# Kernel optimization log

Measured on AMD Instinct MI355X. Metric: run time of the kernel, lower is better.

Reference implementation:

```python
import jax, jax.numpy as jnp
import numpy as np

B, S, D, H = 2, 2048, 1024, 16  # batch, seq, embed_dim, num_heads
DH = D // H                      # head dim = 64


def setup_inputs() -> dict:
    key = jax.random.key(0)
    kx, kq, kbq, kk, kbk, kv, kbv = jax.random.split(key, 7)
    scale = 1.0 / np.sqrt(D)
    return {
        "x": jax.random.normal(kx, (B, S, D), dtype=jnp.float32),
        "Wq": jax.random.normal(kq, (D, D), dtype=jnp.float32) * scale,
        "bq": jax.random.normal(kbq, (D,), dtype=jnp.float32) * 0.01,
        "Wk": jax.random.normal(kk, (D, D), dtype=jnp.float32) * scale,
        "bk": jax.random.normal(kbk, (D,), dtype=jnp.float32) * 0.01,
        "Wv": jax.random.normal(kv, (D, D), dtype=jnp.float32) * scale,
        "bv": jax.random.normal(kbv, (D,), dtype=jnp.float32) * 0.01,
    }


def reference(x, Wq, bq, Wk, bk, Wv, bv):
    # ooqkv_type == 'q', odeint_method == 'id': q branch = act(Linear(x)), exact GELU (torch nn.GELU default)
    q = jax.nn.gelu(x @ Wq + bq, approximate=False)
    k = x @ Wk + bk
    v = x @ Wv + bv
    # [B, S, D] -> [B, S, H, DH]
    q = q.reshape(B, S, H, DH)
    k = k.reshape(B, S, H, DH)
    v = v.reshape(B, S, H, DH)
    # NOTE: original module has NO 1/sqrt(d) scale — faithful reproduction
    att = jnp.einsum("bqhd,bkhd->bhqk", q, k)
    att = jax.nn.softmax(att, axis=-1)
    out = jnp.einsum("bhqk,bkhd->bqhd", att, v)
    return out.reshape(B, S, D)
```

## Files before the change

kernel.cpp:

```cpp
#include <hip/hip_runtime.h>
#include <math.h>

#define B_  2
#define S_  2048
#define D_  1024
#define H_  16
#define DH_ 64
#define M_  (B_ * S_)

typedef _Float16 half_t;
typedef __attribute__((ext_vector_type(8))) _Float16 h8;
typedef __attribute__((ext_vector_type(4))) _Float16 h4;
typedef __attribute__((ext_vector_type(4))) float   f32x4;

#define LOG2E 1.44269504088896f

__device__ __forceinline__ void gll16(const half_t* g, half_t* l) {
    __builtin_amdgcn_global_load_lds(
        (__attribute__((address_space(1))) const void*)g,
        (__attribute__((address_space(3))) void*)l, 16, 0, 0);
}

__global__ __launch_bounds__(256) void prep_k(
    const float* __restrict__ x, half_t* __restrict__ xh,
    const float* __restrict__ Wq, const float* __restrict__ Wk,
    const float* __restrict__ Wv, half_t* __restrict__ Wt)
{
    const int bx = blockIdx.x;
    if (bx < 2048) {
        const size_t i = ((size_t)bx * 256 + threadIdx.x) * 8;
        const float4 a = *(const float4*)(x + i);
        const float4 b = *(const float4*)(x + i + 4);
        h8 o;
        o[0] = (half_t)a.x; o[1] = (half_t)a.y; o[2] = (half_t)a.z; o[3] = (half_t)a.w;
        o[4] = (half_t)b.x; o[5] = (half_t)b.y; o[6] = (half_t)b.z; o[7] = (half_t)b.w;
        *(h8*)(xh + i) = o;
    } else {
        const int gb    = bx - 2048;
        const int which = gb >> 9;
        const float* __restrict__ W = (which == 0) ? Wq : (which == 1) ? Wk : Wv;
        half_t* __restrict__ T = Wt + (size_t)which * D_ * D_;
        const int gw   = (gb & 511) * 4 + (threadIdx.x >> 6);
        const int lane = threadIdx.x & 63;
        const int n    = (gw & 15) * 64 + lane;
        const int k0   = (gw >> 4) * 8;
        h8 o;
        #pragma unroll
        for (int t = 0; t < 8; ++t) o[t] = (half_t)W[(size_t)(k0 + t) * D_ + n];
        *(h8*)(T + (size_t)n * D_ + k0) = o;
    }
}

__global__ __launch_bounds__(256) void qkv_gemm_f16(
    const half_t* __restrict__ xh, const half_t* __restrict__ Wt,
    const float* __restrict__ bq, const float* __restrict__ bk,
    const float* __restrict__ bv,
    half_t* __restrict__ Qo, half_t* __restrict__ Ko, half_t* __restrict__ Vt)
{
    const int n0g   = blockIdx.x * 128;
    const int which = n0g >> 10;
    const int n0    = n0g & 1023;
    const int m0    = blockIdx.y * 128;
    const half_t* __restrict__ Wp  = Wt + (size_t)which * D_ * D_;
    const float* __restrict__ bias = (which == 0) ? bq : (which == 1) ? bk : bv;

    const int tid = threadIdx.x, lane = tid & 63, wave = tid >> 6;
    const int wm = (wave >> 1) * 64, wn = (wave & 1) * 64;
    const int ln = lane & 15, quad = lane >> 4;

    __shared__ __align__(16) half_t As[128 * 64];
    __shared__ __align__(16) half_t Bs[128 * 64];

    f32x4 acc[4][4];
    #pragma unroll
    for (int i = 0; i < 4; ++i)
        #pragma unroll
        for (int j = 0; j < 4; ++j) acc[i][j] = (f32x4){0.f, 0.f, 0.f, 0.f};

    for (int k0 = 0; k0 < D_; k0 += 64) {
        __syncthreads();
        #pragma unroll
        for (int l = 0; l < 4; ++l) {
            const int c  = tid + l * 256;
            const int r  = c >> 3, c0 = c & 7;
            const int cs = c0 ^ (r & 7);
            gll16(xh + (size_t)(m0 + r) * D_ + k0 + cs * 8, &As[c * 8]);
            gll16(Wp + (size_t)(n0 + r) * D_ + k0 + cs * 8, &Bs[c * 8]);
        }
        __syncthreads();

        #pragma unroll
        for (int kc = 0; kc < 2; ++kc) {
            h8 af[4], bf[4];
            #pragma unroll
            for (int i = 0; i < 4; ++i) {
                const int r = wm + i * 16 + ln;
                af[i] = *(const h8*)&As[r * 64 + (((kc << 2) + quad) ^ (r & 7)) * 8];
            }
            #pragma unroll
            for (int j = 0; j < 4; ++j) {
                const int r = wn + j * 16 + ln;
                bf[j] = *(const h8*)&Bs[r * 64 + (((kc << 2) + quad) ^ (r & 7)) * 8];
            }
            #pragma unroll
            for (int i = 0; i < 4; ++i)
                #pragma unroll
                for (int j = 0; j < 4; ++j)
                    acc[i][j] = __builtin_amdgcn_mfma_f32_16x16x32_f16(
                        af[i], bf[j], acc[i][j], 0, 0, 0);
        }
    }

    if (which == 2) {
        #pragma unroll
        for (int j = 0; j < 4; ++j) {
            const int col = n0 + wn + j * 16 + ln;
            const int h = col >> 6, d = col & 63;
            const float bb = bias[col];
            #pragma unroll
            for (int i = 0; i < 4; ++i) {
                const int sg = m0 + wm + i * 16 + quad * 4;
                const int b  = sg >> 11, srow = sg & 2047;
                h4 pv;
                #pragma unroll
                for (int r = 0; r < 4; ++r) pv[r] = (half_t)(acc[i][j][r] + bb);
                *(h4*)(Vt + (((size_t)(b * H_ + h) * DH_ + d) * S_ + srow)) = pv;
            }
        }
    } else {
        half_t* __restrict__ out = (which == 0) ? Qo : Ko;
        #pragma unroll
        for (int j = 0; j < 4; ++j) {
            const int col = n0 + wn + j * 16 + ln;
            const float bb = bias[col];
            #pragma unroll
            for (int i = 0; i < 4; ++i) {
                #pragma unroll
                for (int r = 0; r < 4; ++r) {
                    const int row = m0 + wm + i * 16 + quad * 4 + r;
                    float t = acc[i][j][r] + bb;
                    if (which == 0) {
                        const float u = t * fmaf(t * t, 0.0356774081f, 0.7978845608f);
                        const float e = __builtin_amdgcn_exp2f(u * -2.88539008178f);
                        t = t * __builtin_amdgcn_rcpf(1.0f + e) * LOG2E;
                    }
                    out[(size_t)row * D_ + col] = (half_t)t;
                }
            }
        }
    }
}

__global__ __launch_bounds__(512) void attn_f16(
    const half_t* __restrict__ Q, const half_t* __restrict__ K,
    const half_t* __restrict__ Vt, float* __restrict__ out)
{
    const int tid  = threadIdx.x;
    const int lane = tid & 63;
    const int wave = tid >> 6;
    const int ln   = lane & 15;
    const int quad = lane >> 4;
    const int bh   = blockIdx.y;
    const int b    = bh >> 4;
    const int h    = bh & 15;
    const int q0   = blockIdx.x * 128;

    const half_t* __restrict__ Qb  = Q  + (size_t)b * S_ * D_ + h * DH_;
    const half_t* __restrict__ Kb  = K  + (size_t)b * S_ * D_ + h * DH_;
    const half_t* __restrict__ Vtb = Vt + (size_t)bh * DH_ * S_;

    __shared__ __align__(16) half_t Ks[64 * 64];
    __shared__ __align__(16) half_t Vs[64 * 64];
    __shared__ __align__(16) half_t QPs[128][72];

    {
    }
    const int sr  = tid >> 3, sc0 = tid & 7;
    const int scs = sc0 ^ (sr & 7);
    const half_t* kSrc = Kb  + (size_t)sr * D_ + scs * 8;
    const half_t* vSrc = Vtb + (size_t)sr * S_ + scs * 8;
    half_t* const kDst = &Ks[tid * 8];
    half_t* const vDst = &Vs[tid * 8];

    #pragma unroll
    for (int l = 0; l < 2; ++l) {
        const int c = tid + l * 512;
        const int r = c >> 3, k8 = c & 7;
        *(h8*)&QPs[r][k8 * 8] = *(const h8*)(Qb + (size_t)(q0 + r) * D_ + k8 * 8);
    }
    __syncthreads();
    const h8 qa0 = *(const h8*)&QPs[wave * 16 + ln][quad * 8];
    const h8 qa1 = *(const h8*)&QPs[wave * 16 + ln][32 + quad * 8];

    h8 ones8;
    #pragma unroll
    for (int t = 0; t < 8; ++t) ones8[t] = (half_t)1.0f;

    f32x4 Oa[4];
    #pragma unroll
    for (int j = 0; j < 4; ++j) Oa[j] = (f32x4){0.f, 0.f, 0.f, 0.f};
    f32x4 la = (f32x4){0.f, 0.f, 0.f, 0.f};
    float m_a = -INFINITY;

    for (int k0 = 0; k0 < S_; k0 += 64) {
        __syncthreads();
        gll16(kSrc, kDst);
        gll16(vSrc, vDst);
        kSrc += 64 * D_;
        vSrc += 64;
        __syncthreads();

        f32x4 sa[4];
        __builtin_amdgcn_s_setprio(1);
        #pragma unroll
        for (int j = 0; j < 4; ++j) {
            const int rK = j * 16 + ln;
            const h8 ka0 = *(const h8*)&Ks[rK * 64 + ((quad)     ^ (rK & 7)) * 8];
            const h8 ka1 = *(const h8*)&Ks[rK * 64 + ((quad + 4) ^ (rK & 7)) * 8];
            f32x4 t = (f32x4){0.f, 0.f, 0.f, 0.f};
            t = __builtin_amdgcn_mfma_f32_16x16x32_f16(ka0, qa0, t, 0, 0, 0);
            t = __builtin_amdgcn_mfma_f32_16x16x32_f16(ka1, qa1, t, 0, 0, 0);
            sa[j] = t;
        }
        __builtin_amdgcn_s_setprio(0);

        float mxa = sa[0][0];
        #pragma unroll
        for (int j = 0; j < 4; ++j)
            #pragma unroll
            for (int r = 0; r < 4; ++r) mxa = fmaxf(mxa, sa[j][r]);
        mxa = fmaxf(mxa, __shfl_xor(mxa, 16, 64));
        mxa = fmaxf(mxa, __shfl_xor(mxa, 32, 64));

        if (__ballot(mxa > m_a)) {
            const float mna = fmaxf(m_a, mxa);
            const float ala = __builtin_amdgcn_exp2f(m_a - mna);
            m_a = mna;
            float ra[4];
            #pragma unroll
            for (int r = 0; r < 4; ++r) ra[r] = __shfl(ala, quad * 4 + r, 64);
            #pragma unroll
            for (int r = 0; r < 4; ++r) {
                la[r] *= ra[r];
                #pragma unroll
                for (int j = 0; j < 4; ++j) Oa[j][r] *= ra[r];
            }
        }

        #pragma unroll
        for (int j = 0; j < 4; ++j) {
            h4 pva;
            #pragma unroll
            for (int r = 0; r < 4; ++r)
                pva[r] = (half_t)__builtin_amdgcn_exp2f(sa[j][r] - m_a);
            *(h4*)&QPs[wave * 16 + ln][j * 16 + quad * 4] = pva;
        }

        const h8 pa0 = *(const h8*)&QPs[wave * 16 + ln][quad * 8];
        const h8 pa1 = *(const h8*)&QPs[wave * 16 + ln][32 + quad * 8];
        __builtin_amdgcn_s_setprio(1);
        #pragma unroll
        for (int j = 0; j < 4; ++j) {
            const int rV = j * 16 + ln;
            const h8 vb0 = *(const h8*)&Vs[rV * 64 + ((quad)     ^ (rV & 7)) * 8];
            const h8 vb1 = *(const h8*)&Vs[rV * 64 + ((quad + 4) ^ (rV & 7)) * 8];
            Oa[j] = __builtin_amdgcn_mfma_f32_16x16x32_f16(pa0, vb0, Oa[j], 0, 0, 0);
            Oa[j] = __builtin_amdgcn_mfma_f32_16x16x32_f16(pa1, vb1, Oa[j], 0, 0, 0);
        }
        la = __builtin_amdgcn_mfma_f32_16x16x32_f16(pa0, ones8, la, 0, 0, 0);
        la = __builtin_amdgcn_mfma_f32_16x16x32_f16(pa1, ones8, la, 0, 0, 0);
        __builtin_amdgcn_s_setprio(0);
    }

    #pragma unroll
    for (int r = 0; r < 4; ++r) {
        const float iva = 1.0f / la[r];
        const int rowa = q0 + wave * 16 + quad * 4 + r;
        #pragma unroll
        for (int j = 0; j < 4; ++j)
            out[((size_t)b * S_ + rowa) * D_ + h * DH_ + j * 16 + ln] = Oa[j][r] * iva;
    }
}

extern "C" void kernel_launch(void* const* d_in, const int* in_sizes, int n_in,
                              void* d_out, int out_size, void* d_ws, size_t ws_size,
                              hipStream_t stream) {
    const float* x  = (const float*)d_in[0];
    const float* Wq = (const float*)d_in[1];
    const float* bq = (const float*)d_in[2];
    const float* Wk = (const float*)d_in[3];
    const float* bk = (const float*)d_in[4];
    const float* Wv = (const float*)d_in[5];
    const float* bv = (const float*)d_in[6];
    float* out = (float*)d_out;

    const size_t nmd = (size_t)M_ * D_;
    const size_t ndd = (size_t)D_ * D_;
    half_t* xh  = (half_t*)d_ws;
    half_t* Wt  = xh + nmd;
    half_t* Qh  = Wt + 3 * ndd;
    half_t* Kh  = Qh + nmd;
    half_t* Vtw = Kh + nmd;

    prep_k<<<2048 + 1536, 256, 0, stream>>>(x, xh, Wq, Wk, Wv, Wt);
    qkv_gemm_f16<<<dim3(3 * D_ / 128, M_ / 128), 256, 0, stream>>>(
        xh, Wt, bq, bk, bv, Qh, Kh, Vtw);
    attn_f16<<<dim3(S_ / 128, B_ * H_), 512, 0, stream>>>(Qh, Kh, Vtw, out);
}
```

Measured before the change: 186.5 us.

## Double-buffer K/V tiles in attention kernel to overlap loads with compute

Splits the K/V shared-memory tiles into two ping-pong buffers and issues the async global-to-LDS load for the next tile before computing on the current one. This removes the serial load-then-wait step at the start of each key block, so memory latency can hide behind the MFMA and softmax work. The tile body moves into a macro that is invoked twice per unrolled iteration. In exchange it uses an extra 16 KB of LDS per block, which could lower occupancy, and the loop is hardcoded to 16 double-iterations.

```diff
diff --git a/kernel.cpp b/kernel.cpp
--- a/kernel.cpp
+++ b/kernel.cpp
@@ -151,6 +151,66 @@
     }
 }
 
+#define ATTN_TILE(KS, VS)                                                     \
+    do {                                                                      \
+        f32x4 sa[4];                                                          \
+        __builtin_amdgcn_s_setprio(1);                                        \
+        _Pragma("unroll")                                                     \
+        for (int j = 0; j < 4; ++j) {                                         \
+            const int rK = j * 16 + ln;                                       \
+            const h8 ka0 = *(const h8*)&KS[rK * 64 + ((quad)     ^ (rK & 7)) * 8]; \
+            const h8 ka1 = *(const h8*)&KS[rK * 64 + ((quad + 4) ^ (rK & 7)) * 8]; \
+            f32x4 t = (f32x4){0.f, 0.f, 0.f, 0.f};                            \
+            t = __builtin_amdgcn_mfma_f32_16x16x32_f16(ka0, qa0, t, 0, 0, 0); \
+            t = __builtin_amdgcn_mfma_f32_16x16x32_f16(ka1, qa1, t, 0, 0, 0); \
+            sa[j] = t;                                                        \
+        }                                                                     \
+        __builtin_amdgcn_s_setprio(0);                                        \
+        float mxa = sa[0][0];                                                 \
+        _Pragma("unroll")                                                     \
+        for (int j = 0; j < 4; ++j)                                           \
+            _Pragma("unroll")                                                 \
+            for (int r = 0; r < 4; ++r) mxa = fmaxf(mxa, sa[j][r]);           \
+        mxa = fmaxf(mxa, __shfl_xor(mxa, 16, 64));                            \
+        mxa = fmaxf(mxa, __shfl_xor(mxa, 32, 64));                            \
+        if (__ballot(mxa > m_a)) {                                            \
+            const float mna = fmaxf(m_a, mxa);                                \
+            const float ala = __builtin_amdgcn_exp2f(m_a - mna);              \
+            m_a = mna;                                                        \
+            float ra[4];                                                      \
+            _Pragma("unroll")                                                 \
+            for (int r = 0; r < 4; ++r) ra[r] = __shfl(ala, quad * 4 + r, 64);\
+            _Pragma("unroll")                                                 \
+            for (int r = 0; r < 4; ++r) {                                     \
+                la[r] *= ra[r];                                               \
+                _Pragma("unroll")                                             \
+                for (int j = 0; j < 4; ++j) Oa[j][r] *= ra[r];                \
+            }                                                                 \
+        }                                                                     \
+        _Pragma("unroll")                                                     \
+        for (int j = 0; j < 4; ++j) {                                         \
+            h4 pva;                                                           \
+            _Pragma("unroll")                                                 \
+            for (int r = 0; r < 4; ++r)                                       \
+                pva[r] = (half_t)__builtin_amdgcn_exp2f(sa[j][r] - m_a);      \
+            *(h4*)&QPs[wave * 16 + ln][j * 16 + quad * 4] = pva;              \
+        }                                                                     \
+        const h8 pa0 = *(const h8*)&QPs[wave * 16 + ln][quad * 8];            \
+        const h8 pa1 = *(const h8*)&QPs[wave * 16 + ln][32 + quad * 8];       \
+        __builtin_amdgcn_s_setprio(1);                                        \
+        _Pragma("unroll")                                                     \
+        for (int j = 0; j < 4; ++j) {                                         \
+            const int rV = j * 16 + ln;                                       \
+            const h8 vb0 = *(const h8*)&VS[rV * 64 + ((quad)     ^ (rV & 7)) * 8]; \
+            const h8 vb1 = *(const h8*)&VS[rV * 64 + ((quad + 4) ^ (rV & 7)) * 8]; \
+            Oa[j] = __builtin_amdgcn_mfma_f32_16x16x32_f16(pa0, vb0, Oa[j], 0, 0, 0); \
+            Oa[j] = __builtin_amdgcn_mfma_f32_16x16x32_f16(pa1, vb1, Oa[j], 0, 0, 0); \
+        }                                                                     \
+        la = __builtin_amdgcn_mfma_f32_16x16x32_f16(pa0, ones8, la, 0, 0, 0); \
+        la = __builtin_amdgcn_mfma_f32_16x16x32_f16(pa1, ones8, la, 0, 0, 0); \
+        __builtin_amdgcn_s_setprio(0);                                        \
+    } while (0)
+
 __global__ __launch_bounds__(512) void attn_f16(
     const half_t* __restrict__ Q, const half_t* __restrict__ K,
     const half_t* __restrict__ Vt, float* __restrict__ out)
@@ -169,18 +229,23 @@
     const half_t* __restrict__ Kb  = K  + (size_t)b * S_ * D_ + h * DH_;
     const half_t* __restrict__ Vtb = Vt + (size_t)bh * DH_ * S_;
 
-    __shared__ __align__(16) half_t Ks[64 * 64];
-    __shared__ __align__(16) half_t Vs[64 * 64];
+    __shared__ __align__(16) half_t Ks0[64 * 64];
+    __shared__ __align__(16) half_t Vs0[64 * 64];
+    __shared__ __align__(16) half_t Ks1[64 * 64];
+    __shared__ __align__(16) half_t Vs1[64 * 64];
     __shared__ __align__(16) half_t QPs[128][72];
 
-    {
-    }
     const int sr  = tid >> 3, sc0 = tid & 7;
     const int scs = sc0 ^ (sr & 7);
-    const half_t* kSrc = Kb  + (size_t)sr * D_ + scs * 8;
-    const half_t* vSrc = Vtb + (size_t)sr * S_ + scs * 8;
-    half_t* const kDst = &Ks[tid * 8];
-    half_t* const vDst = &Vs[tid * 8];
+    const half_t* kS = Kb  + (size_t)sr * D_ + scs * 8;
+    const half_t* vS = Vtb + (size_t)sr * S_ + scs * 8;
+    half_t* const kD0 = &Ks0[tid * 8];
+    half_t* const vD0 = &Vs0[tid * 8];
+    half_t* const kD1 = &Ks1[tid * 8];
+    half_t* const vD1 = &Vs1[tid * 8];
+
+    gll16(kS, kD0); gll16(vS, vD0);
+    kS += 64 * D_; vS += 64;
 
     #pragma unroll
     for (int l = 0; l < 2; ++l) {
@@ -202,74 +267,18 @@
     f32x4 la = (f32x4){0.f, 0.f, 0.f, 0.f};
     float m_a = -INFINITY;
 
-    for (int k0 = 0; k0 < S_; k0 += 64) {
+    for (int it = 0; it < 16; ++it) {
+        gll16(kS, kD1); gll16(vS, vD1);
+        kS += 64 * D_; vS += 64;
+        ATTN_TILE(Ks0, Vs0);
         __syncthreads();
-        gll16(kSrc, kDst);
-        gll16(vSrc, vDst);
-        kSrc += 64 * D_;
-        vSrc += 64;
+
+        if (it < 15) {
+            gll16(kS, kD0); gll16(vS, vD0);
+            kS += 64 * D_; vS += 64;
+        }
+        ATTN_TILE(Ks1, Vs1);
         __syncthreads();
-
-        f32x4 sa[4];
-        __builtin_amdgcn_s_setprio(1);
-        #pragma unroll
-        for (int j = 0; j < 4; ++j) {
-            const int rK = j * 16 + ln;
-            const h8 ka0 = *(const h8*)&Ks[rK * 64 + ((quad)     ^ (rK & 7)) * 8];
-            const h8 ka1 = *(const h8*)&Ks[rK * 64 + ((quad + 4) ^ (rK & 7)) * 8];
-            f32x4 t = (f32x4){0.f, 0.f, 0.f, 0.f};
-            t = __builtin_amdgcn_mfma_f32_16x16x32_f16(ka0, qa0, t, 0, 0, 0);
-            t = __builtin_amdgcn_mfma_f32_16x16x32_f16(ka1, qa1, t, 0, 0, 0);
-            sa[j] = t;
-        }
-        __builtin_amdgcn_s_setprio(0);
-
-        float mxa = sa[0][0];
-        #pragma unroll
-        for (int j = 0; j < 4; ++j)
-            #pragma unroll
-            for (int r = 0; r < 4; ++r) mxa = fmaxf(mxa, sa[j][r]);
-        mxa = fmaxf(mxa, __shfl_xor(mxa, 16, 64));
-        mxa = fmaxf(mxa, __shfl_xor(mxa, 32, 64));
-
-        if (__ballot(mxa > m_a)) {
-            const float mna = fmaxf(m_a, mxa);
-            const float ala = __builtin_amdgcn_exp2f(m_a - mna);
-            m_a = mna;
-            float ra[4];
-            #pragma unroll
-            for (int r = 0; r < 4; ++r) ra[r] = __shfl(ala, quad * 4 + r, 64);
-            #pragma unroll
-            for (int r = 0; r < 4; ++r) {
-                la[r] *= ra[r];
-                #pragma unroll
-                for (int j = 0; j < 4; ++j) Oa[j][r] *= ra[r];
-            }
-        }
-
-        #pragma unroll
-        for (int j = 0; j < 4; ++j) {
-            h4 pva;
-            #pragma unroll
-            for (int r = 0; r < 4; ++r)
-                pva[r] = (half_t)__builtin_amdgcn_exp2f(sa[j][r] - m_a);
-            *(h4*)&QPs[wave * 16 + ln][j * 16 + quad * 4] = pva;
-        }
-
-        const h8 pa0 = *(const h8*)&QPs[wave * 16 + ln][quad * 8];
-        const h8 pa1 = *(const h8*)&QPs[wave * 16 + ln][32 + quad * 8];
-        __builtin_amdgcn_s_setprio(1);
-        #pragma unroll
-        for (int j = 0; j < 4; ++j) {
-            const int rV = j * 16 + ln;
-            const h8 vb0 = *(const h8*)&Vs[rV * 64 + ((quad)     ^ (rV & 7)) * 8];
-            const h8 vb1 = *(const h8*)&Vs[rV * 64 + ((quad + 4) ^ (rV & 7)) * 8];
-            Oa[j] = __builtin_amdgcn_mfma_f32_16x16x32_f16(pa0, vb0, Oa[j], 0, 0, 0);
-            Oa[j] = __builtin_amdgcn_mfma_f32_16x16x32_f16(pa1, vb1, Oa[j], 0, 0, 0);
-        }
-        la = __builtin_amdgcn_mfma_f32_16x16x32_f16(pa0, ones8, la, 0, 0, 0);
-        la = __builtin_amdgcn_mfma_f32_16x16x32_f16(pa1, ones8, la, 0, 0, 0);
-        __builtin_amdgcn_s_setprio(0);
     }
 
     #pragma unroll
```

After: 180.2 us. 1.04x faster.

## Swizzle block order for XCD locality and halve attention block size

Applied to the files above, without the earlier changes.

Both the QKV GEMM and the attention kernel now remap linear block IDs with a stride-8 swizzle. The intent is that consecutive blocks landing on the same XCD share A/B or K/V tiles in L2. The attention kernel drops from 512 to 256 threads with 64 queries per block, so twice as many blocks run and each thread loads two K/V chunks per tile. GEMM address arithmetic is hoisted out of the k loop. The risk is more total K/V traffic per query, since each block streams the full K/V for fewer queries.

```diff
diff --git a/kernel.cpp b/kernel.cpp
--- a/kernel.cpp
+++ b/kernel.cpp
@@ -57,10 +57,12 @@
     const float* __restrict__ bv,
     half_t* __restrict__ Qo, half_t* __restrict__ Ko, half_t* __restrict__ Vt)
 {
-    const int n0g   = blockIdx.x * 128;
+    const int lin = blockIdx.y * 24 + blockIdx.x;
+    const int swz = (lin & 7) * 96 + (lin >> 3);
+    const int n0g = (swz % 24) * 128;
+    const int m0  = (swz / 24) * 128;
     const int which = n0g >> 10;
     const int n0    = n0g & 1023;
-    const int m0    = blockIdx.y * 128;
     const half_t* __restrict__ Wp  = Wt + (size_t)which * D_ * D_;
     const float* __restrict__ bias = (which == 0) ? bq : (which == 1) ? bk : bv;
 
@@ -71,6 +73,11 @@
     __shared__ __align__(16) half_t As[128 * 64];
     __shared__ __align__(16) half_t Bs[128 * 64];
 
+    const int r0  = tid >> 3, c0 = tid & 7;
+    const int cs  = c0 ^ (r0 & 7);
+    const half_t* aS = xh + (size_t)(m0 + r0) * D_ + cs * 8;
+    const half_t* bS = Wp + (size_t)(n0 + r0) * D_ + cs * 8;
+
     f32x4 acc[4][4];
     #pragma unroll
     for (int i = 0; i < 4; ++i)
@@ -81,12 +88,10 @@
         __syncthreads();
         #pragma unroll
         for (int l = 0; l < 4; ++l) {
-            const int c  = tid + l * 256;
-            const int r  = c >> 3, c0 = c & 7;
-            const int cs = c0 ^ (r & 7);
-            gll16(xh + (size_t)(m0 + r) * D_ + k0 + cs * 8, &As[c * 8]);
-            gll16(Wp + (size_t)(n0 + r) * D_ + k0 + cs * 8, &Bs[c * 8]);
-        }
+            gll16(aS + (size_t)l * 32 * D_, &As[(tid + l * 256) * 8]);
+            gll16(bS + (size_t)l * 32 * D_, &Bs[(tid + l * 256) * 8]);
+        }
+        aS += 64; bS += 64;
         __syncthreads();
 
         #pragma unroll
@@ -151,7 +156,7 @@
     }
 }
 
-__global__ __launch_bounds__(512) void attn_f16(
+__global__ __launch_bounds__(256) void attn_f16(
     const half_t* __restrict__ Q, const half_t* __restrict__ K,
     const half_t* __restrict__ Vt, float* __restrict__ out)
 {
@@ -160,10 +165,13 @@
     const int wave = tid >> 6;
     const int ln   = lane & 15;
     const int quad = lane >> 4;
-    const int bh   = blockIdx.y;
-    const int b    = bh >> 4;
-    const int h    = bh & 15;
-    const int q0   = blockIdx.x * 128;
+
+    const int lin = blockIdx.y * 32 + blockIdx.x;
+    const int swz = (lin & 7) * 128 + (lin >> 3);
+    const int bh  = swz >> 5;
+    const int b   = bh >> 4;
+    const int h   = bh & 15;
+    const int q0  = (swz & 31) * 64;
 
     const half_t* __restrict__ Qb  = Q  + (size_t)b * S_ * D_ + h * DH_;
     const half_t* __restrict__ Kb  = K  + (size_t)b * S_ * D_ + h * DH_;
@@ -171,20 +179,20 @@
 
     __shared__ __align__(16) half_t Ks[64 * 64];
     __shared__ __align__(16) half_t Vs[64 * 64];
-    __shared__ __align__(16) half_t QPs[128][72];
-
-    {
-    }
+    __shared__ __align__(16) half_t QPs[64][72];
+
     const int sr  = tid >> 3, sc0 = tid & 7;
     const int scs = sc0 ^ (sr & 7);
-    const half_t* kSrc = Kb  + (size_t)sr * D_ + scs * 8;
-    const half_t* vSrc = Vtb + (size_t)sr * S_ + scs * 8;
-    half_t* const kDst = &Ks[tid * 8];
-    half_t* const vDst = &Vs[tid * 8];
+    const half_t* kS = Kb  + (size_t)sr * D_ + scs * 8;
+    const half_t* vS = Vtb + (size_t)sr * S_ + scs * 8;
+    half_t* const kD0 = &Ks[tid * 8];
+    half_t* const kD1 = &Ks[(tid + 256) * 8];
+    half_t* const vD0 = &Vs[tid * 8];
+    half_t* const vD1 = &Vs[(tid + 256) * 8];
 
     #pragma unroll
     for (int l = 0; l < 2; ++l) {
-        const int c = tid + l * 512;
+        const int c = tid + l * 256;
         const int r = c >> 3, k8 = c & 7;
         *(h8*)&QPs[r][k8 * 8] = *(const h8*)(Qb + (size_t)(q0 + r) * D_ + k8 * 8);
     }
@@ -204,10 +212,12 @@
 
     for (int k0 = 0; k0 < S_; k0 += 64) {
         __syncthreads();
-        gll16(kSrc, kDst);
-        gll16(vSrc, vDst);
-        kSrc += 64 * D_;
-        vSrc += 64;
+        gll16(kS,            kD0);
+        gll16(kS + 32 * D_,  kD1);
+        gll16(vS,            vD0);
+        gll16(vS + 32 * S_,  vD1);
+        kS += 64 * D_;
+        vS += 64;
         __syncthreads();
 
         f32x4 sa[4];
@@ -305,5 +315,5 @@
     prep_k<<<2048 + 1536, 256, 0, stream>>>(x, xh, Wq, Wk, Wv, Wt);
     qkv_gemm_f16<<<dim3(3 * D_ / 128, M_ / 128), 256, 0, stream>>>(
         xh, Wt, bq, bk, bv, Qh, Kh, Vtw);
-    attn_f16<<<dim3(S_ / 128, B_ * H_), 512, 0, stream>>>(Qh, Kh, Vtw, out);
-}
+    attn_f16<<<dim3(S_ / 64, B_ * H_), 256, 0, stream>>>(Qh, Kh, Vtw, out);
+}
```

Result: no change. 188.4 us (+1.0%).
